# Kernel tuning notes

Hardware: AMD Instinct MI355X
Metric: run time of the kernel (lower is better)

The kernel has to match this reference:

```python
import jax, jax.numpy as jnp
import numpy as np

EMB_DIM = 512          # hidden_dim d (complex dim); entity rows are 2*d
NUM_ENTITIES = 30000
GAMMA = 12.0
PHASE_RANGE = (GAMMA + 2.0) / EMB_DIM  # self.range in the torch module


def setup_inputs() -> dict:
    key = jax.random.key(0)
    k1, k2, k3, k4 = jax.random.split(key, 4)
    B = 8
    all_h = jax.random.randint(k1, (B,), 0, NUM_ENTITIES, dtype=jnp.int64 if jax.config.x64_enabled else jnp.int32)
    all_r = jax.random.randint(k2, (B,), 0, 1000, dtype=jnp.int64 if jax.config.x64_enabled else jnp.int32)
    eemb = jax.random.normal(k3, (NUM_ENTITIES, 2 * EMB_DIM), dtype=jnp.float32)
    remb = jax.random.normal(k4, (1000, EMB_DIM), dtype=jnp.float32)
    return {"all_h": all_h, "all_r": all_r, "eemb": eemb, "remb": remb}


def reference(all_h, all_r, eemb, remb):
    pi = 3.141592653589793
    # gather query embeddings
    h = eemb[all_h]                       # (B, 2d)
    re_h, im_h = jnp.split(h, 2, axis=-1)  # (B, d) each
    # project relation phases -> unit complex rotation
    phase = remb[all_r] / (PHASE_RANGE / pi)  # (B, d)
    re_r, im_r = jnp.cos(phase), jnp.sin(phase)
    # complex product h * r (rotation), once per query
    re_e = re_h * re_r - im_h * im_r      # (B, d)
    im_e = re_h * im_r + im_h * re_r      # (B, d)
    # distance to ALL entities: |h*r - t| summed over complex components
    re_t, im_t = jnp.split(eemb, 2, axis=-1)  # (N, d) each
    re_diff = re_e[:, None, :] - re_t[None, :, :]  # (B, N, d)
    im_diff = im_e[:, None, :] - im_t[None, :, :]  # (B, N, d)
    dist = jnp.sqrt(re_diff * re_diff + im_diff * im_diff).sum(axis=-1)  # (B, N)
    return GAMMA - dist
```

## Files before the change

kernel.cpp:

```cpp
#include <hip/hip_runtime.h>
#include <math.h>

#define EMB_DIM 512
#define N_Q 8
#define GAMMA_F 12.0f

__global__ __launch_bounds__(256, 2) void rotate_fused_kernel(
    const int* __restrict__ all_h,
    const int* __restrict__ all_r,
    const float* __restrict__ eemb,
    const float* __restrict__ remb,
    float* __restrict__ out,
    int N)
{
    __shared__ float lq[2 * N_Q * EMB_DIM];

    const int tid = threadIdx.x;

    const float SCALE = (float)(M_PI * (double)EMB_DIM / 14.0);
    #pragma unroll
    for (int k = 0; k < 16; ++k) {
        int p = tid + 256 * k;
        int b = p >> 9;
        int j = p & (EMB_DIM - 1);
        int h = all_h[b];
        int r = all_r[b];
        float re_h = eemb[(size_t)h * (2 * EMB_DIM) + j];
        float im_h = eemb[(size_t)h * (2 * EMB_DIM) + EMB_DIM + j];
        float phase = remb[r * EMB_DIM + j] * SCALE;
        float s, c;
        sincosf(phase, &s, &c);
        lq[p]                 = re_h * c - im_h * s;
        lq[N_Q * EMB_DIM + p] = re_h * s + im_h * c;
    }
    __syncthreads();

    const int lane = tid & 63;

    float4 qrA[8], qrB[8], qiA[8], qiB[8];
    #pragma unroll
    for (int b = 0; b < 8; ++b) {
        const float* qb = lq + b * EMB_DIM + 4 * lane;
        qrA[b] = *(const float4*)(qb);
        qrB[b] = *(const float4*)(qb + 256);
        qiA[b] = *(const float4*)(qb + N_Q * EMB_DIM);
        qiB[b] = *(const float4*)(qb + N_Q * EMB_DIM + 256);
    }

    const int wid = tid >> 6;
    int n = blockIdx.x * 4 + wid;
    const int nw = gridDim.x * 4;
    if (n >= N) return;

    const float* base = eemb + 4 * lane;

    float4 rA, rB, iA, iB, nrA, nrB, niA, niB;
    {
        const float* row = base + (size_t)n * (2 * EMB_DIM);
        rA = *(const float4*)(row);
        rB = *(const float4*)(row + 256);
        iA = *(const float4*)(row + 512);
        iB = *(const float4*)(row + 768);
    }

    while (true) {
        int nn = n + nw;
        bool more = nn < N;
        if (more) {
            const float* row = base + (size_t)nn * (2 * EMB_DIM);
            nrA = *(const float4*)(row);
            nrB = *(const float4*)(row + 256);
            niA = *(const float4*)(row + 512);
            niB = *(const float4*)(row + 768);
        }

        float acc[8];
        #pragma unroll
        for (int b = 0; b < 8; ++b) {
            float s = 0.f, dx, dy;
            dx = qrA[b].x - rA.x; dy = qiA[b].x - iA.x; s += __builtin_amdgcn_sqrtf(fmaf(dx, dx, dy * dy));
            dx = qrA[b].y - rA.y; dy = qiA[b].y - iA.y; s += __builtin_amdgcn_sqrtf(fmaf(dx, dx, dy * dy));
            dx = qrA[b].z - rA.z; dy = qiA[b].z - iA.z; s += __builtin_amdgcn_sqrtf(fmaf(dx, dx, dy * dy));
            dx = qrA[b].w - rA.w; dy = qiA[b].w - iA.w; s += __builtin_amdgcn_sqrtf(fmaf(dx, dx, dy * dy));
            dx = qrB[b].x - rB.x; dy = qiB[b].x - iB.x; s += __builtin_amdgcn_sqrtf(fmaf(dx, dx, dy * dy));
            dx = qrB[b].y - rB.y; dy = qiB[b].y - iB.y; s += __builtin_amdgcn_sqrtf(fmaf(dx, dx, dy * dy));
            dx = qrB[b].z - rB.z; dy = qiB[b].z - iB.z; s += __builtin_amdgcn_sqrtf(fmaf(dx, dx, dy * dy));
            dx = qrB[b].w - rB.w; dy = qiB[b].w - iB.w; s += __builtin_amdgcn_sqrtf(fmaf(dx, dx, dy * dy));
            acc[b] = s;
        }

        const bool p1 = lane & 1;
        float r0, r1, r2, r3;
        {
            float x, z;
            x = p1 ? acc[1] : acc[0]; z = p1 ? acc[0] : acc[1]; r0 = x + __shfl_xor(z, 1);
            x = p1 ? acc[3] : acc[2]; z = p1 ? acc[2] : acc[3]; r1 = x + __shfl_xor(z, 1);
            x = p1 ? acc[5] : acc[4]; z = p1 ? acc[4] : acc[5]; r2 = x + __shfl_xor(z, 1);
            x = p1 ? acc[7] : acc[6]; z = p1 ? acc[6] : acc[7]; r3 = x + __shfl_xor(z, 1);
        }
        const bool p2 = lane & 2;
        float t0, t1;
        {
            float x, z;
            x = p2 ? r1 : r0; z = p2 ? r0 : r1; t0 = x + __shfl_xor(z, 2);
            x = p2 ? r3 : r2; z = p2 ? r2 : r3; t1 = x + __shfl_xor(z, 2);
        }
        const bool p3 = lane & 4;
        float u;
        {
            float x, z;
            x = p3 ? t1 : t0; z = p3 ? t0 : t1; u = x + __shfl_xor(z, 4);
        }
        u += __shfl_xor(u, 8);
        u += __shfl_xor(u, 16);
        u += __shfl_xor(u, 32);

        if (lane < 8) out[(size_t)lane * N + n] = GAMMA_F - u;

        if (!more) break;
        n = nn;
        rA = nrA; rB = nrB; iA = niA; iB = niB;
    }
}

extern "C" void kernel_launch(void* const* d_in, const int* in_sizes, int n_in,
                              void* d_out, int out_size, void* d_ws, size_t ws_size,
                              hipStream_t stream) {
    const int*   all_h = (const int*)d_in[0];
    const int*   all_r = (const int*)d_in[1];
    const float* eemb  = (const float*)d_in[2];
    const float* remb  = (const float*)d_in[3];
    float* out = (float*)d_out;

    int N = in_sizes[2] / (2 * EMB_DIM);

    rotate_fused_kernel<<<512, 256, 0, stream>>>(all_h, all_r, eemb, remb, out, N);
}
```

Measured before the change: 191.2 us.

## Split each entity row across two waves to halve query registers, raise occupancy

Each wave now handles half of an entity's embedding dimension, so it holds 8 query float4 pairs instead of 16. This is meant to cut register pressure and allow 4 blocks per CU, with the grid doubled to 1024 blocks. Partial distances from the two waves are combined through shared memory, which adds a __syncthreads per iteration. The query setup also switches to the fast __sincosf intrinsic, which may lose accuracy for large phases.

```diff
diff --git a/kernel.cpp b/kernel.cpp
--- a/kernel.cpp
+++ b/kernel.cpp
@@ -5,7 +5,7 @@
 #define N_Q 8
 #define GAMMA_F 12.0f
 
-__global__ __launch_bounds__(256, 2) void rotate_fused_kernel(
+__global__ __launch_bounds__(256, 4) void rotate_fused_kernel(
     const int* __restrict__ all_h,
     const int* __restrict__ all_r,
     const float* __restrict__ eemb,
@@ -14,6 +14,7 @@
     int N)
 {
     __shared__ float lq[2 * N_Q * EMB_DIM];
+    __shared__ float part[2][4][N_Q];
 
     const int tid = threadIdx.x;
 
@@ -29,81 +30,77 @@
         float im_h = eemb[(size_t)h * (2 * EMB_DIM) + EMB_DIM + j];
         float phase = remb[r * EMB_DIM + j] * SCALE;
         float s, c;
-        sincosf(phase, &s, &c);
+        __sincosf(phase, &s, &c);
         lq[p]                 = re_h * c - im_h * s;
         lq[N_Q * EMB_DIM + p] = re_h * s + im_h * c;
     }
     __syncthreads();
 
     const int lane = tid & 63;
+    const int wid  = tid >> 6;
+    const int half = wid & 1;
+    const int eoff = wid >> 1;
 
-    float4 qrA[8], qrB[8], qiA[8], qiB[8];
+    float4 qr[N_Q], qi[N_Q];
     #pragma unroll
-    for (int b = 0; b < 8; ++b) {
-        const float* qb = lq + b * EMB_DIM + 4 * lane;
-        qrA[b] = *(const float4*)(qb);
-        qrB[b] = *(const float4*)(qb + 256);
-        qiA[b] = *(const float4*)(qb + N_Q * EMB_DIM);
-        qiB[b] = *(const float4*)(qb + N_Q * EMB_DIM + 256);
+    for (int b = 0; b < N_Q; ++b) {
+        const float* qb = lq + b * EMB_DIM + half * 256 + 4 * lane;
+        qr[b] = *(const float4*)(qb);
+        qi[b] = *(const float4*)(qb + N_Q * EMB_DIM);
     }
 
-    const int wid = tid >> 6;
-    int n = blockIdx.x * 4 + wid;
-    const int nw = gridDim.x * 4;
-    if (n >= N) return;
+    const int base0  = blockIdx.x * 2;
+    const int stride = gridDim.x * 2;
+    const int iters  = (N - base0 + stride - 1) / stride;
 
-    const float* base = eemb + 4 * lane;
+    const float* base_re = eemb + half * 256 + 4 * lane;
+    const float* base_im = base_re + EMB_DIM;
 
-    float4 rA, rB, iA, iB, nrA, nrB, niA, niB;
+    float4 r0, i0, nr, ni;
     {
-        const float* row = base + (size_t)n * (2 * EMB_DIM);
-        rA = *(const float4*)(row);
-        rB = *(const float4*)(row + 256);
-        iA = *(const float4*)(row + 512);
-        iB = *(const float4*)(row + 768);
+        int n = base0 + eoff;
+        int nc = (n < N) ? n : 0;
+        const float* p = base_re + (size_t)nc * (2 * EMB_DIM);
+        r0 = *(const float4*)(p);
+        i0 = *(const float4*)(p + EMB_DIM);
     }
 
-    while (true) {
-        int nn = n + nw;
-        bool more = nn < N;
-        if (more) {
-            const float* row = base + (size_t)nn * (2 * EMB_DIM);
-            nrA = *(const float4*)(row);
-            nrB = *(const float4*)(row + 256);
-            niA = *(const float4*)(row + 512);
-            niB = *(const float4*)(row + 768);
+    for (int it = 0; it < iters; ++it) {
+        int n  = base0 + eoff + it * stride;
+        {
+            int n2 = n + stride;
+            int nc = (n2 < N) ? n2 : 0;
+            const float* p = base_re + (size_t)nc * (2 * EMB_DIM);
+            nr = *(const float4*)(p);
+            ni = *(const float4*)(p + EMB_DIM);
         }
 
-        float acc[8];
+        float acc[N_Q];
         #pragma unroll
-        for (int b = 0; b < 8; ++b) {
+        for (int b = 0; b < N_Q; ++b) {
             float s = 0.f, dx, dy;
-            dx = qrA[b].x - rA.x; dy = qiA[b].x - iA.x; s += __builtin_amdgcn_sqrtf(fmaf(dx, dx, dy * dy));
-            dx = qrA[b].y - rA.y; dy = qiA[b].y - iA.y; s += __builtin_amdgcn_sqrtf(fmaf(dx, dx, dy * dy));
-            dx = qrA[b].z - rA.z; dy = qiA[b].z - iA.z; s += __builtin_amdgcn_sqrtf(fmaf(dx, dx, dy * dy));
-            dx = qrA[b].w - rA.w; dy = qiA[b].w - iA.w; s += __builtin_amdgcn_sqrtf(fmaf(dx, dx, dy * dy));
-            dx = qrB[b].x - rB.x; dy = qiB[b].x - iB.x; s += __builtin_amdgcn_sqrtf(fmaf(dx, dx, dy * dy));
-            dx = qrB[b].y - rB.y; dy = qiB[b].y - iB.y; s += __builtin_amdgcn_sqrtf(fmaf(dx, dx, dy * dy));
-            dx = qrB[b].z - rB.z; dy = qiB[b].z - iB.z; s += __builtin_amdgcn_sqrtf(fmaf(dx, dx, dy * dy));
-            dx = qrB[b].w - rB.w; dy = qiB[b].w - iB.w; s += __builtin_amdgcn_sqrtf(fmaf(dx, dx, dy * dy));
+            dx = qr[b].x - r0.x; dy = qi[b].x - i0.x; s += __builtin_amdgcn_sqrtf(fmaf(dx, dx, dy * dy));
+            dx = qr[b].y - r0.y; dy = qi[b].y - i0.y; s += __builtin_amdgcn_sqrtf(fmaf(dx, dx, dy * dy));
+            dx = qr[b].z - r0.z; dy = qi[b].z - i0.z; s += __builtin_amdgcn_sqrtf(fmaf(dx, dx, dy * dy));
+            dx = qr[b].w - r0.w; dy = qi[b].w - i0.w; s += __builtin_amdgcn_sqrtf(fmaf(dx, dx, dy * dy));
             acc[b] = s;
         }
 
         const bool p1 = lane & 1;
-        float r0, r1, r2, r3;
+        float u0, u1, u2, u3;
         {
             float x, z;
-            x = p1 ? acc[1] : acc[0]; z = p1 ? acc[0] : acc[1]; r0 = x + __shfl_xor(z, 1);
-            x = p1 ? acc[3] : acc[2]; z = p1 ? acc[2] : acc[3]; r1 = x + __shfl_xor(z, 1);
-            x = p1 ? acc[5] : acc[4]; z = p1 ? acc[4] : acc[5]; r2 = x + __shfl_xor(z, 1);
-            x = p1 ? acc[7] : acc[6]; z = p1 ? acc[6] : acc[7]; r3 = x + __shfl_xor(z, 1);
+            x = p1 ? acc[1] : acc[0]; z = p1 ? acc[0] : acc[1]; u0 = x + __shfl_xor(z, 1);
+            x = p1 ? acc[3] : acc[2]; z = p1 ? acc[2] : acc[3]; u1 = x + __shfl_xor(z, 1);
+            x = p1 ? acc[5] : acc[4]; z = p1 ? acc[4] : acc[5]; u2 = x + __shfl_xor(z, 1);
+            x = p1 ? acc[7] : acc[6]; z = p1 ? acc[6] : acc[7]; u3 = x + __shfl_xor(z, 1);
         }
         const bool p2 = lane & 2;
         float t0, t1;
         {
             float x, z;
-            x = p2 ? r1 : r0; z = p2 ? r0 : r1; t0 = x + __shfl_xor(z, 2);
-            x = p2 ? r3 : r2; z = p2 ? r2 : r3; t1 = x + __shfl_xor(z, 2);
+            x = p2 ? u1 : u0; z = p2 ? u0 : u1; t0 = x + __shfl_xor(z, 2);
+            x = p2 ? u3 : u2; z = p2 ? u2 : u3; t1 = x + __shfl_xor(z, 2);
         }
         const bool p3 = lane & 4;
         float u;
@@ -115,11 +112,20 @@
         u += __shfl_xor(u, 16);
         u += __shfl_xor(u, 32);
 
-        if (lane < 8) out[(size_t)lane * N + n] = GAMMA_F - u;
+        if (lane < N_Q) part[it & 1][wid][lane] = u;
+        __syncthreads();
 
-        if (!more) break;
-        n = nn;
-        rA = nrA; rB = nrB; iA = niA; iB = niB;
+        if (tid < 2 * N_Q) {
+            int e = tid >> 3;
+            int b = tid & 7;
+            int ns = base0 + e + it * stride;
+            if (ns < N) {
+                float v = part[it & 1][2 * e][b] + part[it & 1][2 * e + 1][b];
+                out[(size_t)b * N + ns] = GAMMA_F - v;
+            }
+        }
+
+        r0 = nr; i0 = ni;
     }
 }
 
@@ -134,5 +140,5 @@
 
     int N = in_sizes[2] / (2 * EMB_DIM);
 
-    rotate_fused_kernel<<<512, 256, 0, stream>>>(all_h, all_r, eemb, remb, out, N);
+    rotate_fused_kernel<<<1024, 256, 0, stream>>>(all_h, all_r, eemb, remb, out, N);
 }
```

After: 184.8 us. -3.4%, faster.
